# Kernel tuning notes

Measured on AMD Instinct MI355X. Metric: run time of the kernel, lower is better.

The kernel has to match this reference:

```python
import jax, jax.numpy as jnp
from jax import lax
import numpy as np

ALPHA, BETA, DECAY, GAMMA = 0.9, 0.1, 0.9, 0.5
KW = 5  # temporal_window


def setup_inputs() -> dict:
    key = jax.random.key(0)
    k1, k2 = jax.random.split(key)
    B, T, F = 128, 128, 2048
    x = jax.random.normal(k1, (B, T, F), dtype=jnp.float32)
    init_threshold = jnp.array(1.0, dtype=jnp.float32)
    conv_w = jax.random.normal(k2, (1, 1, KW), dtype=jnp.float32) * 0.2  # Conv1d(1,1,KW) weight
    conv_b = jnp.zeros((1,), dtype=jnp.float32)
    spatial_attn = jnp.array([1.0], dtype=jnp.float32)
    return {"x": x, "init_threshold": init_threshold, "conv_w": conv_w,
            "conv_b": conv_b, "spatial_attn": spatial_attn}


def _forward(x, init_threshold, conv_w, conv_b, spatial_attn):
    B, T, F = x.shape
    # --- temporal encoding: Conv1d(1,1,KW,'same') along time, per (batch,feature) ---
    xt = jnp.transpose(x, (0, 2, 1)).reshape(B * F, 1, T)  # [B*F,1,T]
    conv = lax.conv_general_dilated(xt, conv_w, window_strides=(1,), padding='SAME',
                                    dimension_numbers=('NCH', 'OIH', 'NCH'))
    conv = conv + conv_b[None, :, None]
    x = jnp.transpose(conv.reshape(B, F, T), (0, 2, 1))  # [B,T,F]
    # --- spatial attention ---
    w = jax.nn.sigmoid(spatial_attn * x.mean(axis=1, keepdims=True))  # [B,1,F]
    x = x * (1.0 + GAMMA * w)
    # --- LIF recurrence over time ---
    mem0 = jnp.zeros((B, F), dtype=x.dtype)
    thr0 = jnp.broadcast_to(init_threshold, (B, F)).astype(x.dtype)
    hist0 = jnp.zeros((B, 3, F), dtype=x.dtype)
    pi = jnp.float32(np.pi)

    def step(carry, xt):
        mem, thr, hist = carry
        mem = DECAY * mem + xt
        spike = 0.5 * (jnp.arctan(pi * (mem - thr) / 2) / pi + 0.5)  # multi_atan surrogate
        hist = jnp.concatenate([hist[:, 1:], spike[:, None]], axis=1)  # [B,3,F]
        avg = hist.mean(axis=1)  # [B,F]
        new_thr = ALPHA * thr + (1.0 - ALPHA) * init_threshold + BETA * avg
        mem = mem - spike * lax.stop_gradient(new_thr)
        return (mem, new_thr, hist), spike

    (mem, _, _), spikes = lax.scan(step, (mem0, thr0, hist0), jnp.transpose(x, (1, 0, 2)))
    return jnp.transpose(spikes, (1, 0, 2)), mem  # [B,T,F], [B,F]


def reference(x, init_threshold, conv_w, conv_b, spatial_attn):
    return _forward(x, init_threshold, conv_w, conv_b, spatial_attn)
```

## Files before the change

### kernel.cpp

```cpp
#include <hip/hip_runtime.h>
#include <math.h>

constexpr int B = 128, T = 128, F = 2048, KW = 5;
#define ALPHA 0.9f
#define BETA  0.1f
#define DECAY 0.9f
#define GAMMA 0.5f

typedef float v2f __attribute__((ext_vector_type(2)));

__device__ __forceinline__ float atan_fast(float z) {
    float az  = __builtin_fabsf(z);
    float inv = __builtin_amdgcn_rcpf(az);
    bool  big = az > 1.0f;
    float u   = big ? inv : az;
    float u2  = u * u;
    float p   = fmaf(u2, -0.01172120f, 0.05265332f);
    p = fmaf(u2, p, -0.11643287f);
    p = fmaf(u2, p,  0.19354346f);
    p = fmaf(u2, p, -0.33262347f);
    p = fmaf(u2, p,  0.99997726f);
    float r = u * p;
    r = big ? (1.57079632679f - r) : r;
    return copysignf(r, z);
}

__global__ __launch_bounds__(256) void lif_fused_kernel(
    const float* __restrict__ x,
    const float* __restrict__ thr0p,
    const float* __restrict__ convw,
    const float* __restrict__ convb,
    const float* __restrict__ sattn,
    float* __restrict__ out)
{
    const int raw    = blockIdx.x;
    const int xcd    = raw & 7;
    const int slot   = raw >> 3;
    const int b      = xcd * 16 + (slot >> 2);
    const int fchunk = slot & 3;
    const int f      = fchunk * 512 + (int)threadIdx.x * 2;

    const float w0 = convw[0], w1 = convw[1], w2 = convw[2],
                w3 = convw[3], w4 = convw[4];
    const float cb   = convb[0];
    const float thr0 = thr0p[0];
    const float sa   = sattn[0];

    const float* xp = x + (size_t)b * T * F + f;

    v2f s0 = {0.f,0.f}, s1 = {0.f,0.f}, s2 = {0.f,0.f}, s3 = {0.f,0.f},
        s4 = {0.f,0.f}, s5 = {0.f,0.f}, s6 = {0.f,0.f}, s7 = {0.f,0.f};
#pragma unroll 2
    for (int t = 0; t < T; t += 8) {
        v2f v0 = *(const v2f*)(xp + (size_t)(t + 0) * F);
        v2f v1 = *(const v2f*)(xp + (size_t)(t + 1) * F);
        v2f v2 = *(const v2f*)(xp + (size_t)(t + 2) * F);
        v2f v3 = *(const v2f*)(xp + (size_t)(t + 3) * F);
        v2f v4 = *(const v2f*)(xp + (size_t)(t + 4) * F);
        v2f v5 = *(const v2f*)(xp + (size_t)(t + 5) * F);
        v2f v6 = *(const v2f*)(xp + (size_t)(t + 6) * F);
        v2f v7 = *(const v2f*)(xp + (size_t)(t + 7) * F);
        s0 += v0; s1 += v1; s2 += v2; s3 += v3;
        s4 += v4; s5 += v5; s6 += v6; s7 += v7;
    }
    v2f sx = ((s0 + s1) + (s2 + s3)) + ((s4 + s5) + (s6 + s7));

    v2f e0  = *(const v2f*)(xp);
    v2f e1  = *(const v2f*)(xp + (size_t)F);
    v2f em2 = *(const v2f*)(xp + (size_t)(T - 2) * F);
    v2f em1 = *(const v2f*)(xp + (size_t)(T - 1) * F);

    const float W = ((w0 + w1) + (w2 + w3)) + w4;
    v2f csum;
    csum.x = fmaf(W, sx.x, (float)T * cb)
           - (w3 + w4) * e0.x - w4 * e1.x - w0 * em2.x - (w0 + w1) * em1.x;
    csum.y = fmaf(W, sx.y, (float)T * cb)
           - (w3 + w4) * e0.y - w4 * e1.y - w0 * em2.y - (w0 + w1) * em1.y;

    v2f scale;
    {
        float zx = sa * (csum.x * (1.0f / (float)T));
        float zy = sa * (csum.y * (1.0f / (float)T));
        scale.x = 1.0f + GAMMA * (1.0f / (1.0f + expf(-zx)));
        scale.y = 1.0f + GAMMA * (1.0f / (1.0f + expf(-zy)));
    }

    const float PIH    = 1.57079632679f;
    const float INV2PI = 0.15915494309f;
    const float thc    = (1.0f - ALPHA) * thr0;

    v2f mem = {0.f, 0.f};
    v2f thr = {thr0, thr0};
    v2f h1 = {0.f, 0.f}, h2 = {0.f, 0.f};
    v2f a = {0.f, 0.f}, bb = {0.f, 0.f}, c = e0, d = e1;

    float* sp = out + (size_t)b * T * F + f;
    float* mp = out + (size_t)B * T * F + (size_t)b * F + f;

    auto lif_step = [&](int t, v2f e) {
        float cx = fmaf(w0, a.x, fmaf(w1, bb.x, fmaf(w2, c.x,
                   fmaf(w3, d.x, fmaf(w4, e.x, cb)))));
        float cy = fmaf(w0, a.y, fmaf(w1, bb.y, fmaf(w2, c.y,
                   fmaf(w3, d.y, fmaf(w4, e.y, cb)))));
        mem.x = fmaf(DECAY, mem.x, cx * scale.x);
        mem.y = fmaf(DECAY, mem.y, cy * scale.y);
        float spx = fmaf(atan_fast(PIH * (mem.x - thr.x)), INV2PI, 0.25f);
        float spy = fmaf(atan_fast(PIH * (mem.y - thr.y)), INV2PI, 0.25f);
        float avx = (h1.x + h2.x + spx) * (1.0f / 3.0f);
        float avy = (h1.y + h2.y + spy) * (1.0f / 3.0f);
        h1 = h2; h2.x = spx; h2.y = spy;
        thr.x = fmaf(ALPHA, thr.x, fmaf(BETA, avx, thc));
        thr.y = fmaf(ALPHA, thr.y, fmaf(BETA, avy, thc));
        mem.x = fmaf(-spx, thr.x, mem.x);
        mem.y = fmaf(-spy, thr.y, mem.y);
        v2f spv = {spx, spy};
        __builtin_nontemporal_store(spv, (v2f*)(sp + (size_t)t * F));
        a = bb; bb = c; c = d; d = e;
    };

#pragma unroll 8
    for (int t = 0; t < T - 2; ++t) {
        v2f e = *(const v2f*)(xp + (size_t)(t + 2) * F);
        lif_step(t, e);
    }
    lif_step(T - 2, (v2f){0.f, 0.f});
    lif_step(T - 1, (v2f){0.f, 0.f});

    __builtin_nontemporal_store(mem, (v2f*)mp);
}

extern "C" void kernel_launch(void* const* d_in, const int* in_sizes, int n_in,
                              void* d_out, int out_size, void* d_ws, size_t ws_size,
                              hipStream_t stream) {
    const float* x     = (const float*)d_in[0];
    const float* thr0  = (const float*)d_in[1];
    const float* convw = (const float*)d_in[2];
    const float* convb = (const float*)d_in[3];
    const float* sattn = (const float*)d_in[4];
    float* out = (float*)d_out;

    const int total = B * F / 2;
    const int block = 256;
    const int grid  = total / block;

    lif_fused_kernel<<<grid, block, 0, stream>>>(x, thr0, convw, convb, sattn, out);
}
```

Baseline: 252.1 us.

## Split fused LIF kernel into separate scale and recurrence kernels

The single fused kernel, which first reduced x over time to compute the attention scale and then ran the LIF recurrence, is split into two launches. The first kernel writes per-(batch,feature) scales to workspace and the second reads them and runs the recurrence. The XCD-aware block remapping is also dropped in favour of plain linear indexing. This decouples the reduction pass from the serial recurrence, but adds a launch, a workspace round trip, and a second full read of x that may no longer hit L2 locality.

```diff
diff --git a/kernel.cpp b/kernel.cpp
--- a/kernel.cpp
+++ b/kernel.cpp
@@ -25,26 +25,24 @@
     return copysignf(r, z);
 }
 
-__global__ __launch_bounds__(256) void lif_fused_kernel(
+
+__global__ __launch_bounds__(256) void scale_kernel(
     const float* __restrict__ x,
     const float* __restrict__ thr0p,
     const float* __restrict__ convw,
     const float* __restrict__ convb,
     const float* __restrict__ sattn,
-    float* __restrict__ out)
+    float* __restrict__ scalebuf)
 {
-    const int raw    = blockIdx.x;
-    const int xcd    = raw & 7;
-    const int slot   = raw >> 3;
-    const int b      = xcd * 16 + (slot >> 2);
-    const int fchunk = slot & 3;
-    const int f      = fchunk * 512 + (int)threadIdx.x * 2;
+    const int tid   = blockIdx.x * blockDim.x + threadIdx.x;
+    const int fpair = tid & (F / 2 - 1);
+    const int b     = tid >> 10;
+    const int f     = fpair * 2;
 
     const float w0 = convw[0], w1 = convw[1], w2 = convw[2],
                 w3 = convw[3], w4 = convw[4];
-    const float cb   = convb[0];
-    const float thr0 = thr0p[0];
-    const float sa   = sattn[0];
+    const float cb = convb[0];
+    const float sa = sattn[0];
 
     const float* xp = x + (size_t)b * T * F + f;
 
@@ -78,12 +76,33 @@
            - (w3 + w4) * e0.y - w4 * e1.y - w0 * em2.y - (w0 + w1) * em1.y;
 
     v2f scale;
-    {
-        float zx = sa * (csum.x * (1.0f / (float)T));
-        float zy = sa * (csum.y * (1.0f / (float)T));
-        scale.x = 1.0f + GAMMA * (1.0f / (1.0f + expf(-zx)));
-        scale.y = 1.0f + GAMMA * (1.0f / (1.0f + expf(-zy)));
-    }
+    scale.x = 1.0f + GAMMA * (1.0f / (1.0f + expf(-sa * (csum.x * (1.0f/(float)T)))));
+    scale.y = 1.0f + GAMMA * (1.0f / (1.0f + expf(-sa * (csum.y * (1.0f/(float)T)))));
+
+    *(v2f*)(scalebuf + (size_t)b * F + f) = scale;
+}
+
+__global__ __launch_bounds__(256) void lif_kernel(
+    const float* __restrict__ x,
+    const float* __restrict__ thr0p,
+    const float* __restrict__ convw,
+    const float* __restrict__ convb,
+    const float* __restrict__ sattn,
+    const float* __restrict__ scalebuf,
+    float* __restrict__ out)
+{
+    const int tid   = blockIdx.x * blockDim.x + threadIdx.x;
+    const int fpair = tid & (F / 2 - 1);
+    const int b     = tid >> 10;
+    const int f     = fpair * 2;
+
+    const float w0 = convw[0], w1 = convw[1], w2 = convw[2],
+                w3 = convw[3], w4 = convw[4];
+    const float cb   = convb[0];
+    const float thr0 = thr0p[0];
+
+    const float* xp = x + (size_t)b * T * F + f;
+    const v2f scale = *(const v2f*)(scalebuf + (size_t)b * F + f);
 
     const float PIH    = 1.57079632679f;
     const float INV2PI = 0.15915494309f;
@@ -92,6 +111,8 @@
     v2f mem = {0.f, 0.f};
     v2f thr = {thr0, thr0};
     v2f h1 = {0.f, 0.f}, h2 = {0.f, 0.f};
+    v2f e0 = *(const v2f*)(xp);
+    v2f e1 = *(const v2f*)(xp + (size_t)F);
     v2f a = {0.f, 0.f}, bb = {0.f, 0.f}, c = e0, d = e1;
 
     float* sp = out + (size_t)b * T * F + f;
@@ -137,11 +158,13 @@
     const float* convw = (const float*)d_in[2];
     const float* convb = (const float*)d_in[3];
     const float* sattn = (const float*)d_in[4];
-    float* out = (float*)d_out;
+    float* out      = (float*)d_out;
+    float* scalebuf = (float*)d_ws;
 
     const int total = B * F / 2;
     const int block = 256;
     const int grid  = total / block;
 
-    lif_fused_kernel<<<grid, block, 0, stream>>>(x, thr0, convw, convb, sattn, out);
+    scale_kernel<<<grid, block, 0, stream>>>(x, thr0, convw, convb, sattn, scalebuf);
+    lif_kernel<<<grid, block, 0, stream>>>(x, thr0, convw, convb, sattn, scalebuf, out);
 }
```

Result: no change. 252.6 us (+0.2%).
